# Performance work log

Hardware: AMD Instinct MI355X
Metric: run time of the kernel (lower is better)

Reference implementation:

```python
import jax, jax.numpy as jnp
import numpy as np

B, N, H = 32, 1024, 512
DT = 0.1  # euler step size = t[1]-t[0] for torchdiffeq euler on t=[0.0,0.1]

def setup_inputs() -> dict:
    key = jax.random.key(0)
    ks = jax.random.split(key, 8)
    s = 1.0 / np.sqrt(2 * H)
    return {
        "inp": jax.random.normal(ks[0], (B, N, H), jnp.float32),
        "hz": jax.random.normal(ks[1], (B, N, H), jnp.float32),
        # func1: tanh(Linear(2H -> 2H)) ODE dynamics
        "Wf": jax.random.uniform(ks[2], (2 * H, 2 * H), jnp.float32, -s, s),
        "bf": jnp.zeros((2 * H,), jnp.float32),
        # mlp head: Linear(2H,2H) -> ReLU -> Linear(2H,H) -> Tanh
        "W1": jax.random.uniform(ks[3], (2 * H, 2 * H), jnp.float32, -s, s),
        "b1": jnp.zeros((2 * H,), jnp.float32),
        "W2": jax.random.uniform(ks[4], (2 * H, H), jnp.float32, -s, s),
        "b2": jnp.zeros((H,), jnp.float32),
    }

def reference(inp, hz, Wf, bf, W1, b1, W2, b2):
    # h0 = cat([input, hz], -1)  -> [B, N, 2H]
    h = jnp.concatenate([inp, hz], axis=-1)
    def func1(h):  # dh/dt (time-independent dynamics)
        return jnp.tanh(h @ Wf + bf)
    # two odeint calls, each a single fixed euler step over t=[0.0, 0.1]
    for _ in range(2):
        h = h + DT * func1(h)
    # MLP head
    h = jax.nn.relu(h @ W1 + b1)
    h = jnp.tanh(h @ W2 + b2)
    return h  # [B, N, H]
```

## Files before the change

### kernel.cpp

```cpp
#include <hip/hip_runtime.h>
#include <hip/hip_bf16.h>

typedef __attribute__((ext_vector_type(8))) short short8;
typedef __attribute__((ext_vector_type(4))) float floatx4;

__device__ __forceinline__ ushort f2bf(float x) {
    __hip_bfloat16 h = __float2bfloat16(x);
    return __builtin_bit_cast(ushort, h);
}
__device__ __forceinline__ float bf2f(ushort u) {
    __hip_bfloat16 h = __builtin_bit_cast(__hip_bfloat16, u);
    return __bfloat162float(h);
}

__device__ __forceinline__ float fast_tanh(float z) {
    float e = __expf(2.0f * z);
    return 1.0f - 2.0f * __builtin_amdgcn_rcpf(e + 1.0f);
}

__device__ __forceinline__ void gload_lds16(const ushort* g, ushort* l) {
    __builtin_amdgcn_global_load_lds(
        (const __attribute__((address_space(1))) unsigned int*)(const void*)g,
        (__attribute__((address_space(3))) unsigned int*)(void*)l,
        16, 0, 0);
}

__global__ void transpose_bf16(const float* __restrict__ W, ushort* __restrict__ WT,
                               int K, int N) {
    __shared__ float tile[32][33];
    int nb = blockIdx.x * 32, kb = blockIdx.y * 32;
    int tx = threadIdx.x, ty = threadIdx.y;
    #pragma unroll
    for (int j = ty; j < 32; j += 8)
        tile[j][tx] = W[(size_t)(kb + j) * N + nb + tx];
    __syncthreads();
    #pragma unroll
    for (int j = ty; j < 32; j += 8)
        WT[(size_t)(nb + j) * K + kb + tx] = f2bf(tile[tx][j]);
}

__global__ void pack_h0(const float* __restrict__ inp, const float* __restrict__ hz,
                        ushort* __restrict__ h0) {
    const float* src = blockIdx.y ? hz : inp;
    size_t i = ((size_t)blockIdx.x * blockDim.x + threadIdx.x) * 4;
    size_t row = i >> 9;
    int col = (int)(i & 511);
    float4 v = *(const float4*)(src + i);
    ushort4 o;
    o.x = f2bf(v.x); o.y = f2bf(v.y); o.z = f2bf(v.z); o.w = f2bf(v.w);
    *(ushort4*)(h0 + row * 1024 + blockIdx.y * 512 + col) = o;
}

template <int MODE, int NOUT, int NX>
__global__ __launch_bounds__(256, 2) void gemm_ep(
    const ushort* __restrict__ A, const ushort* __restrict__ BT,
    const float* __restrict__ bias,
    ushort* __restrict__ outB, float* __restrict__ outF) {
    constexpr int K = 1024;
    __shared__ ushort As[128 * 32];
    __shared__ ushort Bs[128 * 32];

    const int tid = threadIdx.x;
    const int wave = tid >> 6, lane = tid & 63;

    const int id = blockIdx.x;
    const int nTile = (id >> 3) % NX;
    const int mTile = (id & 7) * 32 + (id >> 3) / NX;
    const int mBase = mTile * 128;
    const int nBase = nTile * 128;
    const int waveM = wave >> 1, waveN = wave & 1;

    const int c0 = wave * 128 + lane;
    const int r0 = c0 >> 2;
    const int q0 = (c0 & 3) ^ ((r0 >> 1) & 3);
    const ushort* ag0 = A + (size_t)(mBase + r0) * K + q0 * 8;
    const ushort* ag1 = A + (size_t)(mBase + r0 + 16) * K + q0 * 8;
    const ushort* bg0 = BT + (size_t)(nBase + r0) * K + q0 * 8;
    const ushort* bg1 = BT + (size_t)(nBase + r0 + 16) * K + q0 * 8;
    ushort* asD0 = As + (wave * 128) * 8;
    ushort* asD1 = As + (wave * 128 + 64) * 8;
    ushort* bsD0 = Bs + (wave * 128) * 8;
    ushort* bsD1 = Bs + (wave * 128 + 64) * 8;

    floatx4 acc[4][4];
    #pragma unroll
    for (int i = 0; i < 4; i++)
        #pragma unroll
        for (int j = 0; j < 4; j++) acc[i][j] = (floatx4)(0.f);

    const int mrow = lane & 15;
    const int g = lane >> 4;
    const int pq = g ^ ((mrow >> 1) & 3);
    const int kqOff = pq * 8;

    for (int k0 = 0; k0 < K; k0 += 32) {
        gload_lds16(ag0 + k0, asD0);
        gload_lds16(ag1 + k0, asD1);
        gload_lds16(bg0 + k0, bsD0);
        gload_lds16(bg1 + k0, bsD1);
        __syncthreads();

        short8 af[4], bfr[4];
        #pragma unroll
        for (int t = 0; t < 4; t++) {
            af[t]  = *(const short8*)(As + (waveM * 64 + t * 16 + mrow) * 32 + kqOff);
            bfr[t] = *(const short8*)(Bs + (waveN * 64 + t * 16 + mrow) * 32 + kqOff);
        }
        #pragma unroll
        for (int mt = 0; mt < 4; mt++)
            #pragma unroll
            for (int nt = 0; nt < 4; nt++)
                acc[mt][nt] = __builtin_amdgcn_mfma_f32_16x16x32_bf16(
                    af[mt], bfr[nt], acc[mt][nt], 0, 0, 0);
        __syncthreads();
    }

    const int col0 = nBase + waveN * 64 + (lane & 15);
    const int row0 = mBase + waveM * 64 + (lane >> 4) * 4;
    #pragma unroll
    for (int mt = 0; mt < 4; mt++) {
        #pragma unroll
        for (int nt = 0; nt < 4; nt++) {
            const int col = col0 + nt * 16;
            const float bv = bias[col];
            #pragma unroll
            for (int r = 0; r < 4; r++) {
                const int row = row0 + mt * 16 + r;
                const float z = acc[mt][nt][r] + bv;
                if (MODE == 1) {
                    float carry = bf2f(A[(size_t)row * K + col]);
                    outB[(size_t)row * NOUT + col] = f2bf(carry + 0.1f * fast_tanh(z));
                } else if (MODE == 2) {
                    outB[(size_t)row * NOUT + col] = f2bf(fmaxf(z, 0.f));
                } else {
                    outF[(size_t)row * NOUT + col] = fast_tanh(z);
                }
            }
        }
    }
}

extern "C" void kernel_launch(void* const* d_in, const int* in_sizes, int n_in,
                              void* d_out, int out_size, void* d_ws, size_t ws_size,
                              hipStream_t stream) {
    const float* inp = (const float*)d_in[0];
    const float* hz  = (const float*)d_in[1];
    const float* Wf  = (const float*)d_in[2];
    const float* bf_ = (const float*)d_in[3];
    const float* W1  = (const float*)d_in[4];
    const float* b1  = (const float*)d_in[5];
    const float* W2  = (const float*)d_in[6];
    const float* b2  = (const float*)d_in[7];
    float* out = (float*)d_out;

    char* ws = (char*)d_ws;
    ushort* WfT  = (ushort*)(ws);
    ushort* W1T  = (ushort*)(ws + (size_t)(2 << 20));
    ushort* W2T  = (ushort*)(ws + (size_t)(4 << 20));
    ushort* bufA = (ushort*)(ws + (size_t)(8 << 20));
    ushort* bufB = (ushort*)(ws + (size_t)(8 << 20) + ((size_t)64 << 20));

    transpose_bf16<<<dim3(32, 32), dim3(32, 8), 0, stream>>>(Wf, WfT, 1024, 1024);
    transpose_bf16<<<dim3(32, 32), dim3(32, 8), 0, stream>>>(W1, W1T, 1024, 1024);
    transpose_bf16<<<dim3(16, 32), dim3(32, 8), 0, stream>>>(W2, W2T, 1024, 512);

    pack_h0<<<dim3((32768 * 512 / 4) / 256, 2), 256, 0, stream>>>(inp, hz, bufA);

    gemm_ep<1, 1024, 8><<<8 * 256, 256, 0, stream>>>(bufA, WfT, bf_, bufB, nullptr);
    gemm_ep<1, 1024, 8><<<8 * 256, 256, 0, stream>>>(bufB, WfT, bf_, bufA, nullptr);
    gemm_ep<2, 1024, 8><<<8 * 256, 256, 0, stream>>>(bufA, W1T, b1, bufB, nullptr);
    gemm_ep<3, 512, 4><<<4 * 256, 256, 0, stream>>>(bufB, W2T, b2, nullptr, out);
}
```

Before: 485.0 us.

## Widen GEMM tiles to 128x256 with 8 waves and fuse prep kernels

The GEMM block grows from 256 to 512 threads and its output tile from 128x128 to 128x256. Each 128-row A tile is now shared by twice as many output columns, which cuts global and LDS traffic for A. The four preprocessing launches (three weight transposes plus the h0 pack) are merged into one kernel to remove launch overhead. In exchange the grid has fewer blocks, each block uses more LDS, and the launch bounds now ask for 4 blocks per CU, which may limit occupancy or push up register pressure.

```diff
diff --git a/kernel.cpp b/kernel.cpp
--- a/kernel.cpp
+++ b/kernel.cpp
@@ -25,62 +25,74 @@
         16, 0, 0);
 }
 
-__global__ void transpose_bf16(const float* __restrict__ W, ushort* __restrict__ WT,
-                               int K, int N) {
+__global__ void prep(const float* __restrict__ inp, const float* __restrict__ hz,
+                     const float* __restrict__ Wf, const float* __restrict__ W1,
+                     const float* __restrict__ W2,
+                     ushort* __restrict__ h0, ushort* __restrict__ WfT,
+                     ushort* __restrict__ W1T, ushort* __restrict__ W2T) {
+    int bid = blockIdx.x;
+    int tid = threadIdx.x;
     __shared__ float tile[32][33];
-    int nb = blockIdx.x * 32, kb = blockIdx.y * 32;
-    int tx = threadIdx.x, ty = threadIdx.y;
-    #pragma unroll
-    for (int j = ty; j < 32; j += 8)
-        tile[j][tx] = W[(size_t)(kb + j) * N + nb + tx];
-    __syncthreads();
-    #pragma unroll
-    for (int j = ty; j < 32; j += 8)
-        WT[(size_t)(nb + j) * K + kb + tx] = f2bf(tile[tx][j]);
-}
-
-__global__ void pack_h0(const float* __restrict__ inp, const float* __restrict__ hz,
-                        ushort* __restrict__ h0) {
-    const float* src = blockIdx.y ? hz : inp;
-    size_t i = ((size_t)blockIdx.x * blockDim.x + threadIdx.x) * 4;
-    size_t row = i >> 9;
-    int col = (int)(i & 511);
-    float4 v = *(const float4*)(src + i);
-    ushort4 o;
-    o.x = f2bf(v.x); o.y = f2bf(v.y); o.z = f2bf(v.z); o.w = f2bf(v.w);
-    *(ushort4*)(h0 + row * 1024 + blockIdx.y * 512 + col) = o;
+    if (bid < 32768) {
+        const float* src = (bid < 16384) ? inp : hz;
+        int half = (bid < 16384) ? 0 : 1;
+        int b = bid - half * 16384;
+        size_t i = ((size_t)b * 256 + tid) * 4;
+        size_t row = i >> 9;
+        int col = (int)(i & 511);
+        float4 v = *(const float4*)(src + i);
+        ushort4 o = make_ushort4(f2bf(v.x), f2bf(v.y), f2bf(v.z), f2bf(v.w));
+        *(ushort4*)(h0 + row * 1024 + half * 512 + col) = o;
+    } else {
+        int t = bid - 32768;
+        const float* W;
+        ushort* WT;
+        int K = 1024, N = 1024;
+        if (t < 1024)      { W = Wf; WT = WfT; }
+        else if (t < 2048) { W = W1; WT = W1T; t -= 1024; }
+        else               { W = W2; WT = W2T; t -= 2048; N = 512; }
+        int tx = tid & 31, ty = tid >> 5;
+        int nb = (t % (N / 32)) * 32, kb = (t / (N / 32)) * 32;
+        #pragma unroll
+        for (int j = ty; j < 32; j += 8)
+            tile[j][tx] = W[(size_t)(kb + j) * N + nb + tx];
+        __syncthreads();
+        #pragma unroll
+        for (int j = ty; j < 32; j += 8)
+            WT[(size_t)(nb + j) * K + kb + tx] = f2bf(tile[tx][j]);
+    }
 }
 
 template <int MODE, int NOUT, int NX>
-__global__ __launch_bounds__(256, 2) void gemm_ep(
+__global__ __launch_bounds__(512, 4) void gemm_ep(
     const ushort* __restrict__ A, const ushort* __restrict__ BT,
     const float* __restrict__ bias,
     ushort* __restrict__ outB, float* __restrict__ outF) {
     constexpr int K = 1024;
     __shared__ ushort As[128 * 32];
-    __shared__ ushort Bs[128 * 32];
+    __shared__ ushort Bs[256 * 32];
 
     const int tid = threadIdx.x;
     const int wave = tid >> 6, lane = tid & 63;
 
     const int id = blockIdx.x;
-    const int nTile = (id >> 3) % NX;
-    const int mTile = (id & 7) * 32 + (id >> 3) / NX;
+    const int inner = id >> 3;
+    const int nTile = inner % NX;
+    const int mTile = (id & 7) * 32 + inner / NX;
     const int mBase = mTile * 128;
-    const int nBase = nTile * 128;
-    const int waveM = wave >> 1, waveN = wave & 1;
+    const int nBase = nTile * 256;
+    const int waveM = wave >> 2;
+    const int waveN = wave & 3;
 
-    const int c0 = wave * 128 + lane;
-    const int r0 = c0 >> 2;
-    const int q0 = (c0 & 3) ^ ((r0 >> 1) & 3);
-    const ushort* ag0 = A + (size_t)(mBase + r0) * K + q0 * 8;
-    const ushort* ag1 = A + (size_t)(mBase + r0 + 16) * K + q0 * 8;
-    const ushort* bg0 = BT + (size_t)(nBase + r0) * K + q0 * 8;
-    const ushort* bg1 = BT + (size_t)(nBase + r0 + 16) * K + q0 * 8;
-    ushort* asD0 = As + (wave * 128) * 8;
-    ushort* asD1 = As + (wave * 128 + 64) * 8;
-    ushort* bsD0 = Bs + (wave * 128) * 8;
-    ushort* bsD1 = Bs + (wave * 128 + 64) * 8;
+    const int ca = wave * 64 + lane;
+    const int ra = ca >> 2;
+    const int qa = (ca & 3) ^ ((ra >> 1) & 3);
+    const ushort* agA = A + (size_t)(mBase + ra) * K + qa * 8;
+    const ushort* bg0 = BT + (size_t)(nBase + ra) * K + qa * 8;
+    const ushort* bg1 = BT + (size_t)(nBase + ra + 128) * K + qa * 8;
+    ushort* asD  = As + (size_t)(wave * 64) * 8;
+    ushort* bsD0 = Bs + (size_t)(wave * 64) * 8;
+    ushort* bsD1 = Bs + (size_t)(wave * 64 + 512) * 8;
 
     floatx4 acc[4][4];
     #pragma unroll
@@ -94,8 +106,7 @@
     const int kqOff = pq * 8;
 
     for (int k0 = 0; k0 < K; k0 += 32) {
-        gload_lds16(ag0 + k0, asD0);
-        gload_lds16(ag1 + k0, asD1);
+        gload_lds16(agA + k0, asD);
         gload_lds16(bg0 + k0, bsD0);
         gload_lds16(bg1 + k0, bsD1);
         __syncthreads();
@@ -160,14 +171,10 @@
     ushort* bufA = (ushort*)(ws + (size_t)(8 << 20));
     ushort* bufB = (ushort*)(ws + (size_t)(8 << 20) + ((size_t)64 << 20));
 
-    transpose_bf16<<<dim3(32, 32), dim3(32, 8), 0, stream>>>(Wf, WfT, 1024, 1024);
-    transpose_bf16<<<dim3(32, 32), dim3(32, 8), 0, stream>>>(W1, W1T, 1024, 1024);
-    transpose_bf16<<<dim3(16, 32), dim3(32, 8), 0, stream>>>(W2, W2T, 1024, 512);
+    prep<<<35328, 256, 0, stream>>>(inp, hz, Wf, W1, W2, bufA, WfT, W1T, W2T);
 
-    pack_h0<<<dim3((32768 * 512 / 4) / 256, 2), 256, 0, stream>>>(inp, hz, bufA);
-
-    gemm_ep<1, 1024, 8><<<8 * 256, 256, 0, stream>>>(bufA, WfT, bf_, bufB, nullptr);
-    gemm_ep<1, 1024, 8><<<8 * 256, 256, 0, stream>>>(bufB, WfT, bf_, bufA, nullptr);
-    gemm_ep<2, 1024, 8><<<8 * 256, 256, 0, stream>>>(bufA, W1T, b1, bufB, nullptr);
-    gemm_ep<3, 512, 4><<<4 * 256, 256, 0, stream>>>(bufB, W2T, b2, nullptr, out);
+    gemm_ep<1, 1024, 4><<<1024, 512, 0, stream>>>(bufA, WfT, bf_, bufB, nullptr);
+    gemm_ep<1, 1024, 4><<<1024, 512, 0, stream>>>(bufB, WfT, bf_, bufA, nullptr);
+    gemm_ep<2, 1024, 4><<<1024, 512, 0, stream>>>(bufA, W1T, b1, bufB, nullptr);
+    gemm_ep<3, 512, 2><<<512, 512, 0, stream>>>(bufB, W2T, b2, nullptr, out);
 }
```

Result: faster. 456.8 us (-5.8%).
